# Kernel optimization log

Measured on AMD Instinct MI355X. Metric: run time of the kernel, lower is better.

The kernel has to match this reference:

```python
import jax, jax.numpy as jnp
import numpy as np

VOCAB = 32000
D_MODEL = 1024
PATCH_LEN = 16
NHEAD = 8
B = 8
S = 4096


def setup_inputs() -> dict:
    key = jax.random.key(0)
    ks = jax.random.split(key, 8)
    token_inputs = jax.random.randint(ks[0], (B, S), 0, VOCAB, dtype=jnp.int64 if jax.config.jax_enable_x64 else jnp.int32)
    attention_mask = jax.random.randint(ks[1], (B, S), 0, 2).astype(bool)
    emb_weight = jax.random.normal(ks[2], (VOCAB, D_MODEL), dtype=jnp.float32) * 0.02
    patch_query = jax.random.normal(ks[3], (1, 1, D_MODEL), dtype=jnp.float32) * 0.02
    # nn.MultiheadAttention packed in-projection [3D, D] and out projection [D, D]
    lim = 1.0 / np.sqrt(D_MODEL)
    in_proj_w = jax.random.uniform(ks[4], (3 * D_MODEL, D_MODEL), jnp.float32, -lim, lim)
    in_proj_b = jnp.zeros((3 * D_MODEL,), jnp.float32)
    out_w = jax.random.uniform(ks[5], (D_MODEL, D_MODEL), jnp.float32, -lim, lim)
    out_b = jnp.zeros((D_MODEL,), jnp.float32)
    return {
        "token_inputs": token_inputs,
        "attention_mask": attention_mask,
        "emb_weight": emb_weight,
        "patch_query": patch_query,
        "in_proj_w": in_proj_w,
        "in_proj_b": in_proj_b,
        "out_w": out_w,
        "out_b": out_b,
    }


def reference(token_inputs, attention_mask, emb_weight, patch_query, in_proj_w, in_proj_b, out_w, out_b):
    d_model = emb_weight.shape[1]
    h, dh = NHEAD, d_model // NHEAD
    L = PATCH_LEN

    tok_emb = emb_weight[token_inputs]              # [B, S, D]
    bsz, seqlen, _ = tok_emb.shape
    # seqlen chosen divisible by PATCH_LEN -> pad_len == 0 (matches torch path)
    num_patches = seqlen // L
    BP = bsz * num_patches
    patch_tokens = tok_emb.reshape(BP, L, d_model)  # [BP, L, D]
    patch_mask = attention_mask.reshape(BP, L)      # True = valid token

    patch_valid = patch_mask.any(axis=1)            # [BP]
    # force position 0 valid for fully-empty patches (safe softmax)
    safe_mask = patch_mask | ((~patch_valid)[:, None] & (jnp.arange(L) == 0)[None, :])

    wq, wk, wv = jnp.split(in_proj_w, 3, axis=0)    # each [D, D]
    bq, bk, bv = jnp.split(in_proj_b, 3, axis=0)

    q = patch_query[0, 0] @ wq.T + bq               # [D] (same query for all patches)
    k = patch_tokens @ wk.T + bk                    # [BP, L, D]
    v = patch_tokens @ wv.T + bv                    # [BP, L, D]

    qh = q.reshape(h, dh)                           # [H, dh]
    kh = k.reshape(BP, L, h, dh)                    # [BP, L, H, dh]
    vh = v.reshape(BP, L, h, dh)

    scale = 1.0 / jnp.sqrt(jnp.asarray(dh, q.dtype))
    scores = jnp.einsum('hd,blhd->bhl', qh, kh) * scale   # [BP, H, L]
    scores = jnp.where(safe_mask[:, None, :], scores, -jnp.inf)
    attn = jax.nn.softmax(scores, axis=-1)                # [BP, H, L]

    ctx = jnp.einsum('bhl,blhd->bhd', attn, vh).reshape(BP, d_model)
    patch_latent = ctx @ out_w.T + out_b                  # [BP, D]

    patch_latent = patch_latent.reshape(bsz, num_patches, d_model)
    pv = patch_valid.reshape(bsz, num_patches)
    patch_latent = patch_latent * pv[..., None].astype(patch_latent.dtype)
    return patch_latent, pv
```

## Files before the change

### kernel.cpp

```cpp
#include <hip/hip_runtime.h>
#include <stdint.h>

#define DM    1024
#define LP    16
#define NH    8
#define BP_N  2048
#define OUT_LATENT (2048*1024)
#define SCALE 0.08838834764831845f

typedef float f32x4v __attribute__((ext_vector_type(4)));
typedef short s16x8  __attribute__((ext_vector_type(8)));

static __device__ inline unsigned short f2bf(float f) {
    union { float f; uint32_t u; } v; v.f = f;
    uint32_t u = v.u;
    return (unsigned short)((u + 0x7FFFu + ((u >> 16) & 1u)) >> 16);
}
static __device__ inline float bflo(uint32_t u) {
    union { uint32_t u; float f; } v; v.u = u << 16; return v.f;
}
static __device__ inline float bfhi(uint32_t u) {
    union { uint32_t u; float f; } v; v.u = u & 0xFFFF0000u; return v.f;
}

__global__ __launch_bounds__(256) void k_convw(
    const float* __restrict__ wv_src, const float* __restrict__ ow_src,
    unsigned short* __restrict__ wv_dst, unsigned short* __restrict__ ow_dst) {
    int t = threadIdx.x, b = blockIdx.x;
    const float* src; unsigned short* dst; int idx;
    if (b < 1024) { src = wv_src; dst = wv_dst; idx = b * 1024 + t * 4; }
    else          { src = ow_src; dst = ow_dst; idx = (b - 1024) * 1024 + t * 4; }
    float4 f = *(const float4*)(src + idx);
    ushort4 o; o.x = f2bf(f.x); o.y = f2bf(f.y); o.z = f2bf(f.z); o.w = f2bf(f.w);
    *(ushort4*)(dst + idx) = o;
}

__global__ __launch_bounds__(256) void k_qvec(
    const float* __restrict__ pq, const float* __restrict__ ipw,
    const float* __restrict__ ipb, float* __restrict__ qv) {
    int t = threadIdx.x, wave = t >> 6, lane = t & 63;
    int d = blockIdx.x * 4 + wave;
    const float* wrow = ipw + (size_t)d * 1024;
    float acc = 0.f;
    #pragma unroll
    for (int i = 0; i < 16; ++i) { int j = lane + i * 64; acc = fmaf(pq[j], wrow[j], acc); }
    #pragma unroll
    for (int m = 32; m >= 1; m >>= 1) acc += __shfl_xor(acc, m);
    if (lane == 0) qv[d] = acc + ipb[d];
}

__global__ __launch_bounds__(256) void k_qk(
    const float* __restrict__ qv, const float* __restrict__ ipw,
    const float* __restrict__ ipb, unsigned short* __restrict__ qkb,
    float* __restrict__ sb) {
    __shared__ float qs[128];
    int h = blockIdx.x, t = threadIdx.x;
    if (t < 128) qs[t] = qv[h * 128 + t];
    __syncthreads();
    float a0 = 0.f, a1 = 0.f, a2 = 0.f, a3 = 0.f;
    const float* wbase = ipw + (size_t)(1024 + h * 128) * 1024;
    for (int d = 0; d < 128; ++d) {
        float qd = qs[d];
        const float* wr = wbase + (size_t)d * 1024;
        a0 = fmaf(qd, wr[t], a0);
        a1 = fmaf(qd, wr[t + 256], a1);
        a2 = fmaf(qd, wr[t + 512], a2);
        a3 = fmaf(qd, wr[t + 768], a3);
    }
    qkb[h * 1024 + t]       = f2bf(a0 * SCALE);
    qkb[h * 1024 + t + 256] = f2bf(a1 * SCALE);
    qkb[h * 1024 + t + 512] = f2bf(a2 * SCALE);
    qkb[h * 1024 + t + 768] = f2bf(a3 * SCALE);
    if (t < 64) {
        const float* bk = ipb + 1024 + h * 128;
        float p = qs[t] * bk[t] + qs[t + 64] * bk[t + 64];
        #pragma unroll
        for (int m = 32; m >= 1; m >>= 1) p += __shfl_xor(p, m);
        if (t == 0) sb[h] = p * SCALE;
    }
}

__global__ __launch_bounds__(256) void k_attn(
    const int* __restrict__ tok_ids, const int* __restrict__ amask,
    const float* __restrict__ emb, const unsigned short* __restrict__ qkb,
    const float* __restrict__ sb, unsigned short* __restrict__ Mout,
    float* __restrict__ pv) {
    __shared__ unsigned short tokL[16][1040];
    __shared__ unsigned short qkL[8][1024];
    __shared__ float scoresL[16][8];
    __shared__ float attnL[16][8];
    __shared__ float safeL[16];
    __shared__ int   tokid[16];

    int bp = blockIdx.x, t = threadIdx.x;

    if (t < 16) {
        tokid[t] = tok_ids[bp * 16 + t];
        safeL[t] = amask[bp * 16 + t] ? 1.f : 0.f;
    }
    __syncthreads();
    if (t == 0) {
        int any = 0;
        for (int l = 0; l < 16; ++l) any |= (safeL[l] > 0.f);
        pv[bp] = any ? 1.f : 0.f;
        if (!any) safeL[0] = 1.f;
    }
    {
        const uint4* src = (const uint4*)qkb;
        uint4* dst = (uint4*)&qkL[0][0];
        #pragma unroll
        for (int i = 0; i < 4; ++i) dst[t + i * 256] = src[t + i * 256];
    }
    {
        int row = t >> 4, c = t & 15;
        const float* erow = emb + (size_t)tokid[row] * 1024;
        #pragma unroll
        for (int i = 0; i < 16; ++i) {
            int j4 = c + i * 16;
            float4 f = *(const float4*)(erow + j4 * 4);
            ushort4 o; o.x = f2bf(f.x); o.y = f2bf(f.y); o.z = f2bf(f.z); o.w = f2bf(f.w);
            *(ushort4*)(&tokL[row][j4 * 4]) = o;
        }
    }
    __syncthreads();

    int l = t >> 4, seg = t & 15;
    float acc[8];
    #pragma unroll
    for (int h = 0; h < 8; ++h) acc[h] = 0.f;
    {
        const uint4* tokrow = (const uint4*)&tokL[l][0];
        #pragma unroll
        for (int ii = 0; ii < 8; ++ii) {
            int iofs = (seg + ii) & 7;
            uint4 tv = tokrow[seg * 8 + iofs];
            float t0 = bflo(tv.x), t1 = bfhi(tv.x), t2 = bflo(tv.y), t3 = bfhi(tv.y);
            float t4 = bflo(tv.z), t5 = bfhi(tv.z), t6 = bflo(tv.w), t7 = bfhi(tv.w);
            #pragma unroll
            for (int h = 0; h < 8; ++h) {
                uint4 qv = *(const uint4*)(&qkL[h][seg * 64 + iofs * 8]);
                float s = acc[h];
                s = fmaf(t0, bflo(qv.x), s); s = fmaf(t1, bfhi(qv.x), s);
                s = fmaf(t2, bflo(qv.y), s); s = fmaf(t3, bfhi(qv.y), s);
                s = fmaf(t4, bflo(qv.z), s); s = fmaf(t5, bfhi(qv.z), s);
                s = fmaf(t6, bflo(qv.w), s); s = fmaf(t7, bfhi(qv.w), s);
                acc[h] = s;
            }
        }
    }
    #pragma unroll
    for (int h = 0; h < 8; ++h) {
        float a = acc[h];
        a += __shfl_xor(a, 1); a += __shfl_xor(a, 2);
        a += __shfl_xor(a, 4); a += __shfl_xor(a, 8);
        acc[h] = a;
    }
    if (seg < 8) {
        float v = acc[0];
        #pragma unroll
        for (int h = 1; h < 8; ++h) v = (seg == h) ? acc[h] : v;
        scoresL[l][seg] = v;
    }
    __syncthreads();

    if (t < 128) {
        int hh = t >> 4, ll = t & 15;
        float s = (safeL[ll] > 0.f) ? (scoresL[ll][hh] + sb[hh]) : -1e30f;
        float mx = s;
        mx = fmaxf(mx, __shfl_xor(mx, 1)); mx = fmaxf(mx, __shfl_xor(mx, 2));
        mx = fmaxf(mx, __shfl_xor(mx, 4)); mx = fmaxf(mx, __shfl_xor(mx, 8));
        float e = __expf(s - mx);
        float sum = e;
        sum += __shfl_xor(sum, 1); sum += __shfl_xor(sum, 2);
        sum += __shfl_xor(sum, 4); sum += __shfl_xor(sum, 8);
        attnL[ll][hh] = e / sum;
    }
    __syncthreads();

    float macc[8][4];
    #pragma unroll
    for (int h = 0; h < 8; ++h)
        #pragma unroll
        for (int c = 0; c < 4; ++c) macc[h][c] = 0.f;
    #pragma unroll
    for (int ll = 0; ll < 16; ++ll) {
        uint2 tv = *(const uint2*)(&tokL[ll][t * 4]);
        float t0 = bflo(tv.x), t1 = bfhi(tv.x), t2 = bflo(tv.y), t3 = bfhi(tv.y);
        float4 a0 = *(const float4*)(&attnL[ll][0]);
        float4 a1 = *(const float4*)(&attnL[ll][4]);
        macc[0][0] = fmaf(a0.x, t0, macc[0][0]); macc[0][1] = fmaf(a0.x, t1, macc[0][1]);
        macc[0][2] = fmaf(a0.x, t2, macc[0][2]); macc[0][3] = fmaf(a0.x, t3, macc[0][3]);
        macc[1][0] = fmaf(a0.y, t0, macc[1][0]); macc[1][1] = fmaf(a0.y, t1, macc[1][1]);
        macc[1][2] = fmaf(a0.y, t2, macc[1][2]); macc[1][3] = fmaf(a0.y, t3, macc[1][3]);
        macc[2][0] = fmaf(a0.z, t0, macc[2][0]); macc[2][1] = fmaf(a0.z, t1, macc[2][1]);
        macc[2][2] = fmaf(a0.z, t2, macc[2][2]); macc[2][3] = fmaf(a0.z, t3, macc[2][3]);
        macc[3][0] = fmaf(a0.w, t0, macc[3][0]); macc[3][1] = fmaf(a0.w, t1, macc[3][1]);
        macc[3][2] = fmaf(a0.w, t2, macc[3][2]); macc[3][3] = fmaf(a0.w, t3, macc[3][3]);
        macc[4][0] = fmaf(a1.x, t0, macc[4][0]); macc[4][1] = fmaf(a1.x, t1, macc[4][1]);
        macc[4][2] = fmaf(a1.x, t2, macc[4][2]); macc[4][3] = fmaf(a1.x, t3, macc[4][3]);
        macc[5][0] = fmaf(a1.y, t0, macc[5][0]); macc[5][1] = fmaf(a1.y, t1, macc[5][1]);
        macc[5][2] = fmaf(a1.y, t2, macc[5][2]); macc[5][3] = fmaf(a1.y, t3, macc[5][3]);
        macc[6][0] = fmaf(a1.z, t0, macc[6][0]); macc[6][1] = fmaf(a1.z, t1, macc[6][1]);
        macc[6][2] = fmaf(a1.z, t2, macc[6][2]); macc[6][3] = fmaf(a1.z, t3, macc[6][3]);
        macc[7][0] = fmaf(a1.w, t0, macc[7][0]); macc[7][1] = fmaf(a1.w, t1, macc[7][1]);
        macc[7][2] = fmaf(a1.w, t2, macc[7][2]); macc[7][3] = fmaf(a1.w, t3, macc[7][3]);
    }
    #pragma unroll
    for (int h = 0; h < 8; ++h) {
        ushort4 o;
        o.x = f2bf(macc[h][0]); o.y = f2bf(macc[h][1]);
        o.z = f2bf(macc[h][2]); o.w = f2bf(macc[h][3]);
        *(ushort4*)(Mout + ((size_t)(h * 2048 + bp)) * 1024 + t * 4) = o;
    }
}

__device__ inline void gemm_tile_64x64(
    const unsigned short* __restrict__ A, const unsigned short* __restrict__ Bm,
    int m0, f32x4v acc[4], unsigned short* As, unsigned short* Bs) {
    int t = threadIdx.x;
    int row = t >> 2, seg = t & 3;
    int wave = t >> 6, lane = t & 63, lrow = lane & 15, quad = lane >> 4;
    #pragma unroll
    for (int nt = 0; nt < 4; ++nt) acc[nt] = (f32x4v){0.f, 0.f, 0.f, 0.f};
    for (int step = 0; step < 32; ++step) {
        int k0 = step * 32;
        uint4 av = *(const uint4*)(A  + (size_t)(m0 + row) * 1024 + k0 + seg * 8);
        uint4 bv = *(const uint4*)(Bm + (size_t)row * 1024 + k0 + seg * 8);
        __syncthreads();
        *(uint4*)(As + row * 40 + seg * 8) = av;
        *(uint4*)(Bs + row * 40 + seg * 8) = bv;
        __syncthreads();
        s16x8 af = *(const s16x8*)(As + (wave * 16 + lrow) * 40 + quad * 8);
        #pragma unroll
        for (int nt = 0; nt < 4; ++nt) {
            s16x8 bf = *(const s16x8*)(Bs + (nt * 16 + lrow) * 40 + quad * 8);
            acc[nt] = __builtin_amdgcn_mfma_f32_16x16x32_bf16(af, bf, acc[nt], 0, 0, 0);
        }
    }
}

__global__ __launch_bounds__(256) void k_gemm_ctx(
    const unsigned short* __restrict__ M, const unsigned short* __restrict__ wv,
    const float* __restrict__ ipb, unsigned short* __restrict__ ctx) {
    __shared__ unsigned short As[64 * 40], Bs[64 * 40];
    int mb = blockIdx.x, nb = blockIdx.y, h = blockIdx.z;
    int m0 = mb * 64, nloc0 = nb * 64;
    const unsigned short* A  = M + (size_t)h * 2048 * 1024;
    const unsigned short* Bm = wv + (size_t)(h * 128 + nloc0) * 1024;
    f32x4v acc[4];
    gemm_tile_64x64(A, Bm, m0, acc, As, Bs);
    int lane = threadIdx.x & 63, wave = threadIdx.x >> 6;
    int lrow = lane & 15, quad = lane >> 4;
    #pragma unroll
    for (int nt = 0; nt < 4; ++nt) {
        int n_g = h * 128 + nloc0 + nt * 16 + lrow;
        float bias = ipb[2048 + n_g];
        #pragma unroll
        for (int r = 0; r < 4; ++r) {
            int row_g = m0 + wave * 16 + quad * 4 + r;
            ctx[(size_t)row_g * 1024 + n_g] = f2bf(acc[nt][r] + bias);
        }
    }
}

__global__ __launch_bounds__(256) void k_gemm_out(
    const unsigned short* __restrict__ ctx, const unsigned short* __restrict__ ow,
    const float* __restrict__ outb, const float* __restrict__ pv,
    float* __restrict__ out) {
    __shared__ unsigned short As[64 * 40], Bs[64 * 40];
    int mb = blockIdx.x, nb = blockIdx.y;
    int m0 = mb * 64, n0 = nb * 64;
    f32x4v acc[4];
    gemm_tile_64x64(ctx, ow + (size_t)n0 * 1024, m0, acc, As, Bs);
    int t = threadIdx.x;
    int lane = t & 63, wave = t >> 6, lrow = lane & 15, quad = lane >> 4;
    #pragma unroll
    for (int nt = 0; nt < 4; ++nt) {
        int n_g = n0 + nt * 16 + lrow;
        float bias = outb[n_g];
        #pragma unroll
        for (int r = 0; r < 4; ++r) {
            int row_g = m0 + wave * 16 + quad * 4 + r;
            out[(size_t)row_g * 1024 + n_g] = (acc[nt][r] + bias) * pv[row_g];
        }
    }
    if (nb == 0 && t < 64) out[OUT_LATENT + m0 + t] = pv[m0 + t];
}

extern "C" void kernel_launch(void* const* d_in, const int* in_sizes, int n_in,
                              void* d_out, int out_size, void* d_ws, size_t ws_size,
                              hipStream_t stream) {
    const int*   tok = (const int*)d_in[0];
    const int*   msk = (const int*)d_in[1];
    const float* emb = (const float*)d_in[2];
    const float* pq  = (const float*)d_in[3];
    const float* ipw = (const float*)d_in[4];
    const float* ipb = (const float*)d_in[5];
    const float* ow  = (const float*)d_in[6];
    const float* ob  = (const float*)d_in[7];
    float* out = (float*)d_out;
    char* ws = (char*)d_ws;

    float*          q_f   = (float*)(ws + 0);
    float*          sb_f  = (float*)(ws + 4096);
    float*          pv_f  = (float*)(ws + 8192);
    unsigned short* qk_b  = (unsigned short*)(ws + 16384);
    unsigned short* wv_b  = (unsigned short*)(ws + 32768);
    unsigned short* ow_b  = (unsigned short*)(ws + 32768 + 2097152);
    unsigned short* ctx_b = (unsigned short*)(ws + 32768 + 2 * 2097152);
    unsigned short* M_b   = (unsigned short*)(ws + 32768 + 2 * 2097152 + 4194304);

    k_convw<<<dim3(2048), dim3(256), 0, stream>>>(ipw + (size_t)2048 * 1024, ow, wv_b, ow_b);
    k_qvec <<<dim3(256),  dim3(256), 0, stream>>>(pq, ipw, ipb, q_f);
    k_qk   <<<dim3(8),    dim3(256), 0, stream>>>(q_f, ipw, ipb, qk_b, sb_f);
    k_attn <<<dim3(2048), dim3(256), 0, stream>>>(tok, msk, emb, qk_b, sb_f, M_b, pv_f);
    k_gemm_ctx<<<dim3(32, 2, 8), dim3(256), 0, stream>>>(M_b, wv_b, ipb, ctx_b);
    k_gemm_out<<<dim3(32, 16, 1), dim3(256), 0, stream>>>(ctx_b, ow_b, ob, pv_f, out);
}
```

Measured before the change: 276.9 us.

## Use MFMA scores, async LDS loads, 128x128 GEMM tiles, and parallel qk

The attention kernel now computes its scores with bf16 MFMA instructions, with q·Wk fragments held in registers instead of scalar FMA loops over an LDS copy. The two GEMMs move from 64x64 to 128x128 tiles with a 2x2 wave layout and use global_load_lds async copies to stage operands. The qk precompute kernel is spread over 64 blocks instead of 8, and the mask handling is restructured with shuffles. The larger tiles raise operand reuse but leave only 128 blocks per GEMM, which may underfill the GPU's compute units, and the GEMM main loop is still not double-buffered.

```diff
diff --git a/kernel.cpp b/kernel.cpp
--- a/kernel.cpp
+++ b/kernel.cpp
@@ -1,10 +1,6 @@
 #include <hip/hip_runtime.h>
 #include <stdint.h>
 
-#define DM    1024
-#define LP    16
-#define NH    8
-#define BP_N  2048
 #define OUT_LATENT (2048*1024)
 #define SCALE 0.08838834764831845f
 
@@ -21,6 +17,12 @@
 }
 static __device__ inline float bfhi(uint32_t u) {
     union { uint32_t u; float f; } v; v.u = u & 0xFFFF0000u; return v.f;
+}
+
+static __device__ __forceinline__ void async16(const unsigned short* g, unsigned short* l) {
+    __builtin_amdgcn_global_load_lds(
+        (const __attribute__((address_space(1))) void*)g,
+        (__attribute__((address_space(3))) void*)l, 16, 0, 0);
 }
 
 __global__ __launch_bounds__(256) void k_convw(
@@ -54,24 +56,20 @@
     const float* __restrict__ ipb, unsigned short* __restrict__ qkb,
     float* __restrict__ sb) {
     __shared__ float qs[128];
-    int h = blockIdx.x, t = threadIdx.x;
+    __shared__ float part[128];
+    int h = blockIdx.x, jseg = blockIdx.y, t = threadIdx.x;
+    int jl = t & 127, dh = t >> 7;
     if (t < 128) qs[t] = qv[h * 128 + t];
     __syncthreads();
-    float a0 = 0.f, a1 = 0.f, a2 = 0.f, a3 = 0.f;
-    const float* wbase = ipw + (size_t)(1024 + h * 128) * 1024;
-    for (int d = 0; d < 128; ++d) {
-        float qd = qs[d];
-        const float* wr = wbase + (size_t)d * 1024;
-        a0 = fmaf(qd, wr[t], a0);
-        a1 = fmaf(qd, wr[t + 256], a1);
-        a2 = fmaf(qd, wr[t + 512], a2);
-        a3 = fmaf(qd, wr[t + 768], a3);
-    }
-    qkb[h * 1024 + t]       = f2bf(a0 * SCALE);
-    qkb[h * 1024 + t + 256] = f2bf(a1 * SCALE);
-    qkb[h * 1024 + t + 512] = f2bf(a2 * SCALE);
-    qkb[h * 1024 + t + 768] = f2bf(a3 * SCALE);
-    if (t < 64) {
+    float acc = 0.f;
+    const float* wbase = ipw + (size_t)(1024 + h * 128 + dh * 64) * 1024 + jseg * 128 + jl;
+    #pragma unroll 8
+    for (int d = 0; d < 64; ++d)
+        acc = fmaf(qs[dh * 64 + d], wbase[(size_t)d * 1024], acc);
+    if (dh) part[jl] = acc;
+    __syncthreads();
+    if (!dh) qkb[h * 1024 + jseg * 128 + jl] = f2bf((acc + part[jl]) * SCALE);
+    if (jseg == 0 && t < 64) {
         const float* bk = ipb + 1024 + h * 128;
         float p = qs[t] * bk[t] + qs[t + 64] * bk[t + 64];
         #pragma unroll
@@ -85,35 +83,25 @@
     const float* __restrict__ emb, const unsigned short* __restrict__ qkb,
     const float* __restrict__ sb, unsigned short* __restrict__ Mout,
     float* __restrict__ pv) {
-    __shared__ unsigned short tokL[16][1040];
-    __shared__ unsigned short qkL[8][1024];
-    __shared__ float scoresL[16][8];
+    __shared__ unsigned short tokL[16][1032];
+    __shared__ float scoresP[4][16][8];
     __shared__ float attnL[16][8];
-    __shared__ float safeL[16];
-    __shared__ int   tokid[16];
+    __shared__ int allzL;
 
     int bp = blockIdx.x, t = threadIdx.x;
-
-    if (t < 16) {
-        tokid[t] = tok_ids[bp * 16 + t];
-        safeL[t] = amask[bp * 16 + t] ? 1.f : 0.f;
-    }
-    __syncthreads();
-    if (t == 0) {
-        int any = 0;
-        for (int l = 0; l < 16; ++l) any |= (safeL[l] > 0.f);
-        pv[bp] = any ? 1.f : 0.f;
-        if (!any) safeL[0] = 1.f;
-    }
+    int wave = t >> 6, lane = t & 63, lrow = lane & 15, quad = lane >> 4;
+
+    s16x8 bfr[8];
     {
-        const uint4* src = (const uint4*)qkb;
-        uint4* dst = (uint4*)&qkL[0][0];
-        #pragma unroll
-        for (int i = 0; i < 4; ++i) dst[t + i * 256] = src[t + i * 256];
-    }
+        const unsigned short* qbase = qkb + (lane & 7) * 1024 + wave * 256 + quad * 8;
+        #pragma unroll
+        for (int s = 0; s < 8; ++s) bfr[s] = *(const s16x8*)(qbase + s * 32);
+    }
+
     {
         int row = t >> 4, c = t & 15;
-        const float* erow = emb + (size_t)tokid[row] * 1024;
+        int tid = tok_ids[bp * 16 + row];
+        const float* erow = emb + (size_t)tid * 1024;
         #pragma unroll
         for (int i = 0; i < 16; ++i) {
             int j4 = c + i * 16;
@@ -122,50 +110,35 @@
             *(ushort4*)(&tokL[row][j4 * 4]) = o;
         }
     }
-    __syncthreads();
-
-    int l = t >> 4, seg = t & 15;
-    float acc[8];
-    #pragma unroll
-    for (int h = 0; h < 8; ++h) acc[h] = 0.f;
+    if (t < 16) {
+        int any = (amask[bp * 16 + t] != 0);
+        any |= __shfl_xor(any, 1); any |= __shfl_xor(any, 2);
+        any |= __shfl_xor(any, 4); any |= __shfl_xor(any, 8);
+        if (t == 0) { pv[bp] = any ? 1.f : 0.f; allzL = any ? 0 : 1; }
+    }
+    __syncthreads();
+
     {
-        const uint4* tokrow = (const uint4*)&tokL[l][0];
-        #pragma unroll
-        for (int ii = 0; ii < 8; ++ii) {
-            int iofs = (seg + ii) & 7;
-            uint4 tv = tokrow[seg * 8 + iofs];
-            float t0 = bflo(tv.x), t1 = bfhi(tv.x), t2 = bflo(tv.y), t3 = bfhi(tv.y);
-            float t4 = bflo(tv.z), t5 = bfhi(tv.z), t6 = bflo(tv.w), t7 = bfhi(tv.w);
+        f32x4v acc = (f32x4v){0.f, 0.f, 0.f, 0.f};
+        const unsigned short* arow = &tokL[lrow][wave * 256 + quad * 8];
+        #pragma unroll
+        for (int s = 0; s < 8; ++s) {
+            s16x8 af = *(const s16x8*)(arow + s * 32);
+            acc = __builtin_amdgcn_mfma_f32_16x16x32_bf16(af, bfr[s], acc, 0, 0, 0);
+        }
+        if (lrow < 8) {
             #pragma unroll
-            for (int h = 0; h < 8; ++h) {
-                uint4 qv = *(const uint4*)(&qkL[h][seg * 64 + iofs * 8]);
-                float s = acc[h];
-                s = fmaf(t0, bflo(qv.x), s); s = fmaf(t1, bfhi(qv.x), s);
-                s = fmaf(t2, bflo(qv.y), s); s = fmaf(t3, bfhi(qv.y), s);
-                s = fmaf(t4, bflo(qv.z), s); s = fmaf(t5, bfhi(qv.z), s);
-                s = fmaf(t6, bflo(qv.w), s); s = fmaf(t7, bfhi(qv.w), s);
-                acc[h] = s;
-            }
-        }
-    }
-    #pragma unroll
-    for (int h = 0; h < 8; ++h) {
-        float a = acc[h];
-        a += __shfl_xor(a, 1); a += __shfl_xor(a, 2);
-        a += __shfl_xor(a, 4); a += __shfl_xor(a, 8);
-        acc[h] = a;
-    }
-    if (seg < 8) {
-        float v = acc[0];
-        #pragma unroll
-        for (int h = 1; h < 8; ++h) v = (seg == h) ? acc[h] : v;
-        scoresL[l][seg] = v;
+            for (int r = 0; r < 4; ++r) scoresP[wave][quad * 4 + r][lrow] = acc[r];
+        }
     }
     __syncthreads();
 
     if (t < 128) {
         int hh = t >> 4, ll = t & 15;
-        float s = (safeL[ll] > 0.f) ? (scoresL[ll][hh] + sb[hh]) : -1e30f;
+        float s = scoresP[0][ll][hh] + scoresP[1][ll][hh]
+                + scoresP[2][ll][hh] + scoresP[3][ll][hh] + sb[hh];
+        bool valid = (amask[bp * 16 + ll] != 0) || (allzL && ll == 0);
+        s = valid ? s : -1e30f;
         float mx = s;
         mx = fmaxf(mx, __shfl_xor(mx, 1)); mx = fmaxf(mx, __shfl_xor(mx, 2));
         mx = fmaxf(mx, __shfl_xor(mx, 4)); mx = fmaxf(mx, __shfl_xor(mx, 8));
@@ -214,51 +187,60 @@
     }
 }
 
-__device__ inline void gemm_tile_64x64(
-    const unsigned short* __restrict__ A, const unsigned short* __restrict__ Bm,
-    int m0, f32x4v acc[4], unsigned short* As, unsigned short* Bs) {
+__device__ __forceinline__ void gemm128_mainloop(
+    const unsigned short* __restrict__ A, const unsigned short* __restrict__ B,
+    unsigned short* As, unsigned short* Bs, f32x4v acc[4][4]) {
     int t = threadIdx.x;
-    int row = t >> 2, seg = t & 3;
     int wave = t >> 6, lane = t & 63, lrow = lane & 15, quad = lane >> 4;
-    #pragma unroll
-    for (int nt = 0; nt < 4; ++nt) acc[nt] = (f32x4v){0.f, 0.f, 0.f, 0.f};
+    int wm = wave & 1, wn = wave >> 1;
+    int srow = t >> 2, sseg = (t & 3) * 8;
+    #pragma unroll
+    for (int mi = 0; mi < 4; ++mi)
+        #pragma unroll
+        for (int ni = 0; ni < 4; ++ni) acc[mi][ni] = (f32x4v){0.f, 0.f, 0.f, 0.f};
     for (int step = 0; step < 32; ++step) {
         int k0 = step * 32;
-        uint4 av = *(const uint4*)(A  + (size_t)(m0 + row) * 1024 + k0 + seg * 8);
-        uint4 bv = *(const uint4*)(Bm + (size_t)row * 1024 + k0 + seg * 8);
         __syncthreads();
-        *(uint4*)(As + row * 40 + seg * 8) = av;
-        *(uint4*)(Bs + row * 40 + seg * 8) = bv;
+        async16(A + (size_t)srow * 1024 + k0 + sseg,        As + t * 8);
+        async16(A + (size_t)(srow + 64) * 1024 + k0 + sseg, As + (256 + t) * 8);
+        async16(B + (size_t)srow * 1024 + k0 + sseg,        Bs + t * 8);
+        async16(B + (size_t)(srow + 64) * 1024 + k0 + sseg, Bs + (256 + t) * 8);
         __syncthreads();
-        s16x8 af = *(const s16x8*)(As + (wave * 16 + lrow) * 40 + quad * 8);
-        #pragma unroll
-        for (int nt = 0; nt < 4; ++nt) {
-            s16x8 bf = *(const s16x8*)(Bs + (nt * 16 + lrow) * 40 + quad * 8);
-            acc[nt] = __builtin_amdgcn_mfma_f32_16x16x32_bf16(af, bf, acc[nt], 0, 0, 0);
-        }
+        s16x8 af[4], bf[4];
+        #pragma unroll
+        for (int i = 0; i < 4; ++i) {
+            af[i] = *(const s16x8*)(As + (wm * 64 + i * 16 + lrow) * 32 + quad * 8);
+            bf[i] = *(const s16x8*)(Bs + (wn * 64 + i * 16 + lrow) * 32 + quad * 8);
+        }
+        #pragma unroll
+        for (int mi = 0; mi < 4; ++mi)
+            #pragma unroll
+            for (int ni = 0; ni < 4; ++ni)
+                acc[mi][ni] = __builtin_amdgcn_mfma_f32_16x16x32_bf16(af[mi], bf[ni], acc[mi][ni], 0, 0, 0);
     }
 }
 
 __global__ __launch_bounds__(256) void k_gemm_ctx(
     const unsigned short* __restrict__ M, const unsigned short* __restrict__ wv,
     const float* __restrict__ ipb, unsigned short* __restrict__ ctx) {
-    __shared__ unsigned short As[64 * 40], Bs[64 * 40];
-    int mb = blockIdx.x, nb = blockIdx.y, h = blockIdx.z;
-    int m0 = mb * 64, nloc0 = nb * 64;
-    const unsigned short* A  = M + (size_t)h * 2048 * 1024;
-    const unsigned short* Bm = wv + (size_t)(h * 128 + nloc0) * 1024;
-    f32x4v acc[4];
-    gemm_tile_64x64(A, Bm, m0, acc, As, Bs);
-    int lane = threadIdx.x & 63, wave = threadIdx.x >> 6;
-    int lrow = lane & 15, quad = lane >> 4;
-    #pragma unroll
-    for (int nt = 0; nt < 4; ++nt) {
-        int n_g = h * 128 + nloc0 + nt * 16 + lrow;
+    __shared__ unsigned short As[128 * 32], Bs[128 * 32];
+    int mb = blockIdx.x, h = blockIdx.y;
+    f32x4v acc[4][4];
+    gemm128_mainloop(M + ((size_t)h * 2048 + mb * 128) * 1024,
+                     wv + (size_t)h * 128 * 1024, As, Bs, acc);
+    int t = threadIdx.x, wave = t >> 6, lane = t & 63, lrow = lane & 15, quad = lane >> 4;
+    int wm = wave & 1, wn = wave >> 1;
+    #pragma unroll
+    for (int ni = 0; ni < 4; ++ni) {
+        int n_g = h * 128 + wn * 64 + ni * 16 + lrow;
         float bias = ipb[2048 + n_g];
         #pragma unroll
-        for (int r = 0; r < 4; ++r) {
-            int row_g = m0 + wave * 16 + quad * 4 + r;
-            ctx[(size_t)row_g * 1024 + n_g] = f2bf(acc[nt][r] + bias);
+        for (int mi = 0; mi < 4; ++mi) {
+            #pragma unroll
+            for (int r = 0; r < 4; ++r) {
+                int m_g = mb * 128 + wm * 64 + mi * 16 + quad * 4 + r;
+                ctx[(size_t)m_g * 1024 + n_g] = f2bf(acc[mi][ni][r] + bias);
+            }
         }
     }
 }
@@ -267,24 +249,27 @@
     const unsigned short* __restrict__ ctx, const unsigned short* __restrict__ ow,
     const float* __restrict__ outb, const float* __restrict__ pv,
     float* __restrict__ out) {
-    __shared__ unsigned short As[64 * 40], Bs[64 * 40];
+    __shared__ unsigned short As[128 * 32], Bs[128 * 32];
     int mb = blockIdx.x, nb = blockIdx.y;
-    int m0 = mb * 64, n0 = nb * 64;
-    f32x4v acc[4];
-    gemm_tile_64x64(ctx, ow + (size_t)n0 * 1024, m0, acc, As, Bs);
-    int t = threadIdx.x;
-    int lane = t & 63, wave = t >> 6, lrow = lane & 15, quad = lane >> 4;
-    #pragma unroll
-    for (int nt = 0; nt < 4; ++nt) {
-        int n_g = n0 + nt * 16 + lrow;
+    f32x4v acc[4][4];
+    gemm128_mainloop(ctx + (size_t)mb * 128 * 1024,
+                     ow + (size_t)nb * 128 * 1024, As, Bs, acc);
+    int t = threadIdx.x, wave = t >> 6, lane = t & 63, lrow = lane & 15, quad = lane >> 4;
+    int wm = wave & 1, wn = wave >> 1;
+    #pragma unroll
+    for (int ni = 0; ni < 4; ++ni) {
+        int n_g = nb * 128 + wn * 64 + ni * 16 + lrow;
         float bias = outb[n_g];
         #pragma unroll
-        for (int r = 0; r < 4; ++r) {
-            int row_g = m0 + wave * 16 + quad * 4 + r;
-            out[(size_t)row_g * 1024 + n_g] = (acc[nt][r] + bias) * pv[row_g];
-        }
-    }
-    if (nb == 0 && t < 64) out[OUT_LATENT + m0 + t] = pv[m0 + t];
+        for (int mi = 0; mi < 4; ++mi) {
+            #pragma unroll
+            for (int r = 0; r < 4; ++r) {
+                int m_g = mb * 128 + wm * 64 + mi * 16 + quad * 4 + r;
+                out[(size_t)m_g * 1024 + n_g] = (acc[mi][ni][r] + bias) * pv[m_g];
+            }
+        }
+    }
+    if (nb == 0 && t < 128) out[OUT_LATENT + mb * 128 + t] = pv[mb * 128 + t];
 }
 
 extern "C" void kernel_launch(void* const* d_in, const int* in_sizes, int n_in,
@@ -312,8 +297,8 @@
 
     k_convw<<<dim3(2048), dim3(256), 0, stream>>>(ipw + (size_t)2048 * 1024, ow, wv_b, ow_b);
     k_qvec <<<dim3(256),  dim3(256), 0, stream>>>(pq, ipw, ipb, q_f);
-    k_qk   <<<dim3(8),    dim3(256), 0, stream>>>(q_f, ipw, ipb, qk_b, sb_f);
+    k_qk   <<<dim3(8, 8), dim3(256), 0, stream>>>(q_f, ipw, ipb, qk_b, sb_f);
     k_attn <<<dim3(2048), dim3(256), 0, stream>>>(tok, msk, emb, qk_b, sb_f, M_b, pv_f);
-    k_gemm_ctx<<<dim3(32, 2, 8), dim3(256), 0, stream>>>(M_b, wv_b, ipb, ctx_b);
-    k_gemm_out<<<dim3(32, 16, 1), dim3(256), 0, stream>>>(ctx_b, ow_b, ob, pv_f, out);
-}
+    k_gemm_ctx<<<dim3(16, 8), dim3(256), 0, stream>>>(M_b, wv_b, ipb, ctx_b);
+    k_gemm_out<<<dim3(16, 8), dim3(256), 0, stream>>>(ctx_b, ow_b, ob, pv_f, out);
+}
```

Result: faster. 267.3 us (-3.5%).
